# Kernel tuning notes

Hardware: AMD Instinct MI355X
Metric: run time of the kernel (lower is better)

## Reference

```python
import jax, jax.numpy as jnp
import numpy as np

N_NODES = 50000
N_EDGES = 500000
CLIP_DIM = 512   # openai/clip-vit-base-patch32 projection_dim
HIDDEN = 512
NUM_CLASSES = 100


def setup_inputs() -> dict:
    key = jax.random.key(0)
    ks = jax.random.split(key, 8)
    x = jax.random.normal(ks[0], (N_NODES, CLIP_DIM), dtype=jnp.float32)
    edge_index = jax.random.randint(ks[1], (2, N_EDGES), 0, N_NODES)
    W1 = jax.random.normal(ks[2], (HIDDEN, CLIP_DIM), dtype=jnp.float32) / np.sqrt(CLIP_DIM)
    b1 = jnp.zeros((HIDDEN,), dtype=jnp.float32)
    W2 = jax.random.normal(ks[3], (HIDDEN, HIDDEN), dtype=jnp.float32) / np.sqrt(HIDDEN)
    b2 = jnp.zeros((HIDDEN,), dtype=jnp.float32)
    Wc = jax.random.normal(ks[4], (NUM_CLASSES, HIDDEN), dtype=jnp.float32) / np.sqrt(HIDDEN)
    bc = jnp.zeros((NUM_CLASSES,), dtype=jnp.float32)
    return {"x": x, "edge_index": edge_index, "W1": W1, "b1": b1,
            "W2": W2, "b2": b2, "Wc": Wc, "bc": bc}


def _gcn_conv(h, W, b, src, dst, coef, n_nodes):
    # PyG GCNConv: transform, then normalized scatter-add aggregation, then bias.
    h = h @ W.T                                   # [N, out]
    msg = h[src] * coef[:, None]                  # [E+N, out] gathered messages
    out = jax.ops.segment_sum(msg, dst, num_segments=n_nodes)
    return out + b


def reference(x, edge_index, W1, b1, W2, b2, Wc, bc):
    n = x.shape[0]
    loop = jnp.arange(n, dtype=edge_index.dtype)
    src = jnp.concatenate([edge_index[0], loop])  # add self-loops (GCN default)
    dst = jnp.concatenate([edge_index[1], loop])
    # symmetric normalization deg^-1/2 on both endpoints (unit edge weights)
    deg = jax.ops.segment_sum(jnp.ones_like(src, dtype=x.dtype), dst, num_segments=n)
    norm = jax.lax.rsqrt(deg)                     # deg >= 1 due to self-loops
    coef = norm[src] * norm[dst]

    h = _gcn_conv(x, W1, b1, src, dst, coef, n)
    h = jax.nn.relu(h)
    # dropout(p=0.2) is identity in eval mode
    h = _gcn_conv(h, W2, b2, src, dst, coef, n)
    h = jax.nn.relu(h)
    return h @ Wc.T + bc                          # [N, num_classes]
```

## Files before the change

### kernel.cpp

```cpp
#include <hip/hip_runtime.h>

#define HIDDEN 512
#define BLK_ELEMS (64 * 128 * 8)

typedef __attribute__((ext_vector_type(8))) short short8;
typedef __attribute__((ext_vector_type(4))) float f32x4;

__device__ __forceinline__ unsigned short f2bf(float f) {
    unsigned u = __float_as_uint(f);
    unsigned r = (u + 0x7FFFu + ((u >> 16) & 1u)) >> 16;
    return (unsigned short)r;
}
__device__ __forceinline__ float bf2f(unsigned short h) {
    return __uint_as_float(((unsigned)h) << 16);
}

__device__ __forceinline__ void load_lds16(const unsigned short* g, unsigned short* l) {
    __builtin_amdgcn_global_load_lds(
        (const __attribute__((address_space(1))) unsigned int*)(g),
        (__attribute__((address_space(3))) unsigned int*)(l), 16, 0, 0);
}

__device__ __forceinline__ void acc8(uint4 v, float cf, float* a) {
    a[0] = fmaf(cf, bf2f((unsigned short)(v.x & 0xFFFF)), a[0]);
    a[1] = fmaf(cf, bf2f((unsigned short)(v.x >> 16)),    a[1]);
    a[2] = fmaf(cf, bf2f((unsigned short)(v.y & 0xFFFF)), a[2]);
    a[3] = fmaf(cf, bf2f((unsigned short)(v.y >> 16)),    a[3]);
    a[4] = fmaf(cf, bf2f((unsigned short)(v.z & 0xFFFF)), a[4]);
    a[5] = fmaf(cf, bf2f((unsigned short)(v.z >> 16)),    a[5]);
    a[6] = fmaf(cf, bf2f((unsigned short)(v.w & 0xFFFF)), a[6]);
    a[7] = fmaf(cf, bf2f((unsigned short)(v.w >> 16)),    a[7]);
}


__device__ __forceinline__ void cast_chunk(const float* __restrict__ src,
                                           unsigned short* __restrict__ dst,
                                           int rows, int o) {
    int blk = o >> 13;
    int rem = o & 8191;
    int g = rem >> 7;
    int m = rem & 127;
    int row = blk * 128 + m;
    short8 v;
    if (row < rows) {
        const float* p = src + (size_t)row * HIDDEN + g * 8;
        float4 f0 = *(const float4*)p;
        float4 f1 = *(const float4*)(p + 4);
        v[0] = (short)f2bf(f0.x); v[1] = (short)f2bf(f0.y);
        v[2] = (short)f2bf(f0.z); v[3] = (short)f2bf(f0.w);
        v[4] = (short)f2bf(f1.x); v[5] = (short)f2bf(f1.y);
        v[6] = (short)f2bf(f1.z); v[7] = (short)f2bf(f1.w);
    } else {
        v = (short8)0;
    }
    *(short8*)(dst + (size_t)o * 8) = v;
}


__global__ __launch_bounds__(256)
void fused_count_castx(const int* __restrict__ dstv, int* __restrict__ cnt, int E, int countB,
                       const float* __restrict__ x, unsigned short* __restrict__ bufA,
                       int rows, int xchunks) {
    int b = blockIdx.x;
    if (b < countB) {
        int e = b * 256 + threadIdx.x;
        if (e < E) atomicAdd(&cnt[dstv[e]], 1);
    } else {
        int o = (b - countB) * 256 + threadIdx.x;
        if (o < xchunks) cast_chunk(x, bufA, rows, o);
    }
}


__global__ __launch_bounds__(256)
void fused_bsum_castw(const int* __restrict__ cnt, float* __restrict__ norm,
                      int* __restrict__ bsums, int n, int NSB,
                      const float* __restrict__ W1, const float* __restrict__ W2,
                      const float* __restrict__ Wc,
                      unsigned short* __restrict__ W1t, unsigned short* __restrict__ W2t,
                      unsigned short* __restrict__ Wct, int NC) {
    __shared__ int red[256];
    int tid = threadIdx.x;
    if ((int)blockIdx.x < NSB) {
        int i = blockIdx.x * 256 + tid;
        int v = 0;
        if (i < n) {
            v = cnt[i];
            norm[i] = rsqrtf((float)(v + 1));
        }
        red[tid] = v;
        __syncthreads();
        #pragma unroll
        for (int off = 128; off > 0; off >>= 1) {
            if (tid < off) red[tid] += red[tid + off];
            __syncthreads();
        }
        if (tid == 0) bsums[blockIdx.x] = red[0];
    } else {
        int o = ((int)blockIdx.x - NSB) * 256 + tid;
        if (o < 32768) {
            cast_chunk(W1, W1t, HIDDEN, o);
        } else if (o < 65536) {
            cast_chunk(W2, W2t, HIDDEN, o - 32768);
        } else if (o < 73728) {
            cast_chunk(Wc, Wct, NC, o - 65536);
        }
    }
}

__global__ __launch_bounds__(256)
void bscan_kernel(const int* __restrict__ bsums, int* __restrict__ boffs,
                  int* __restrict__ rowptr_n, int nb) {
    __shared__ int buf[256];
    int tid = threadIdx.x;
    int v = (tid < nb) ? bsums[tid] : 0;
    buf[tid] = v;
    __syncthreads();
    #pragma unroll
    for (int off = 1; off < 256; off <<= 1) {
        int t = (tid >= off) ? buf[tid - off] : 0;
        __syncthreads();
        buf[tid] += t;
        __syncthreads();
    }
    if (tid < nb) boffs[tid] = buf[tid] - v;
    if (tid == 255) rowptr_n[0] = buf[255];
}

__global__ __launch_bounds__(256)
void scan_final_kernel(const int* __restrict__ cnt, const int* __restrict__ boffs,
                       int* __restrict__ rowptr, int* __restrict__ cursor, int n) {
    __shared__ int buf[256];
    int tid = threadIdx.x;
    int i = blockIdx.x * 256 + tid;
    int v = (i < n) ? cnt[i] : 0;
    buf[tid] = v;
    __syncthreads();
    #pragma unroll
    for (int off = 1; off < 256; off <<= 1) {
        int t = (tid >= off) ? buf[tid - off] : 0;
        __syncthreads();
        buf[tid] += t;
        __syncthreads();
    }
    if (i < n) {
        int ex = boffs[blockIdx.x] + buf[tid] - v;
        rowptr[i] = ex;
        cursor[i] = ex;
    }
}


template<int MODE>
__device__ __forceinline__ void gemm_body(const unsigned short* __restrict__ At,
                                          const unsigned short* __restrict__ Bt,
                                          const float* __restrict__ bias,
                                          void* __restrict__ Cout,
                                          int M, int NC, int mb, int nb) {
    __shared__ __align__(16) unsigned short As[8 * 128 * 8];
    __shared__ __align__(16) unsigned short Bs[8 * 128 * 8];

    const int tid = threadIdx.x;
    const int wid = tid >> 6;
    const int lane = tid & 63;
    const int wm = wid & 1, wn = wid >> 1;
    const int lm = lane & 15;
    const int lq = lane >> 4;

    const unsigned short* Ab = At + (size_t)mb * BLK_ELEMS;
    const unsigned short* Bb = Bt + (size_t)nb * BLK_ELEMS;

    f32x4 acc[4][4];
    #pragma unroll
    for (int i = 0; i < 4; ++i)
        #pragma unroll
        for (int j = 0; j < 4; ++j) acc[i][j] = (f32x4)0.f;

    for (int kt = 0; kt < 8; ++kt) {
        __syncthreads();
        const unsigned short* ga = Ab + kt * (8 * 1024);
        const unsigned short* gb = Bb + kt * (8 * 1024);
        #pragma unroll
        for (int i = 0; i < 4; ++i) {
            int off = (tid + i * 256) * 8;
            load_lds16(ga + off, As + off);
            load_lds16(gb + off, Bs + off);
        }
        __syncthreads();
        #pragma unroll
        for (int ks = 0; ks < 2; ++ks) {
            int g = ks * 4 + lq;
            int base = g * 1024 + lm * 8;
            short8 af[4], bfr[4];
            #pragma unroll
            for (int mt = 0; mt < 4; ++mt)
                af[mt] = *(const short8*)&As[base + (wm * 64 + mt * 16) * 8];
            #pragma unroll
            for (int nt = 0; nt < 4; ++nt)
                bfr[nt] = *(const short8*)&Bs[base + (wn * 64 + nt * 16) * 8];
            #pragma unroll
            for (int mt = 0; mt < 4; ++mt)
                #pragma unroll
                for (int nt = 0; nt < 4; ++nt)
                    acc[mt][nt] = __builtin_amdgcn_mfma_f32_16x16x32_bf16(
                        af[mt], bfr[nt], acc[mt][nt], 0, 0, 0);
        }
    }

    #pragma unroll
    for (int mt = 0; mt < 4; ++mt) {
        #pragma unroll
        for (int nt = 0; nt < 4; ++nt) {
            int col = nb * 128 + wn * 64 + nt * 16 + lm;
            f32x4 v = acc[mt][nt];
            #pragma unroll
            for (int r = 0; r < 4; ++r) {
                int row = mb * 128 + wm * 64 + mt * 16 + lq * 4 + r;
                if (row < M) {
                    if (MODE == 0) {
                        ((unsigned short*)Cout)[(size_t)row * HIDDEN + col] = f2bf(v[r]);
                    } else {
                        if (col < NC)
                            ((float*)Cout)[(size_t)row * NC + col] = v[r] + bias[col];
                    }
                }
            }
        }
    }
}

__device__ __forceinline__ bool swz_decode(int bid, int NB, int& mb, int& nb) {
    int p = bid & 7;
    int s = bid >> 3;
    nb = s & 3;
    mb = (s >> 2) * 8 + p;
    return mb < NB;
}

template<int MODE>
__global__ __launch_bounds__(256)
void gemm_swz(const unsigned short* __restrict__ At, const unsigned short* __restrict__ Bt,
              const float* __restrict__ bias, void* __restrict__ Cout,
              int M, int NC, int NB) {
    int mb, nb;
    if (!swz_decode(blockIdx.x, NB, mb, nb)) return;
    gemm_body<MODE>(At, Bt, bias, Cout, M, NC, mb, nb);
}

template<int MODE>
__global__ __launch_bounds__(256)
void gemm_plain(const unsigned short* __restrict__ At, const unsigned short* __restrict__ Bt,
                const float* __restrict__ bias, void* __restrict__ Cout,
                int M, int NC) {
    gemm_body<MODE>(At, Bt, bias, Cout, M, NC, blockIdx.x, blockIdx.y);
}


__global__ __launch_bounds__(256)
void fused_fill_gemm1(const int* __restrict__ src, const int* __restrict__ dstv,
                      const float* __restrict__ norm, int* __restrict__ cursor,
                      int2* __restrict__ epair, int E, int fillB,
                      const unsigned short* __restrict__ At, const unsigned short* __restrict__ Bt,
                      void* __restrict__ Cout, int M, int NB) {
    int b = blockIdx.x;
    if (b < fillB) {
        int e = b * 256 + threadIdx.x;
        if (e < E) {
            int s = src[e], d = dstv[e];
            float cf = norm[s] * norm[d];
            int p = atomicAdd(&cursor[d], 1);
            epair[p] = make_int2(s, __float_as_int(cf));
        }
    } else {
        int mb, nb;
        if (swz_decode(b - fillB, NB, mb, nb))
            gemm_body<0>(At, Bt, nullptr, Cout, M, HIDDEN, mb, nb);
    }
}


__global__ __launch_bounds__(256)
void aggregate_kernel(const unsigned short* __restrict__ h, const int* __restrict__ rowptr,
                      const int2* __restrict__ epair, const float* __restrict__ norm,
                      const float* __restrict__ bias, unsigned short* __restrict__ out_t,
                      int N) {
    const int wave = threadIdx.x >> 6;
    const int lane = threadIdx.x & 63;
    const int node = blockIdx.x * 4 + wave;
    if (node >= N) return;
    const uint4* h4 = (const uint4*)h;
    const int c = lane;

    float a[8];
    {
        uint4 sv = h4[(size_t)node * 64 + c];
        float nv = norm[node];
        float invd = nv * nv;
        a[0] = a[1] = a[2] = a[3] = a[4] = a[5] = a[6] = a[7] = 0.f;
        acc8(sv, invd, a);
    }

    int beg = rowptr[node], end = rowptr[node + 1];
    int j = beg;
    if ((j & 1) && j < end) {
        int2 p = epair[j];
        uint4 v = h4[(size_t)p.x * 64 + c];
        acc8(v, __int_as_float(p.y), a);
        ++j;
    }
    for (; j + 8 <= end; j += 8) {
        int4 q0 = *(const int4*)(epair + j);
        int4 q1 = *(const int4*)(epair + j + 2);
        int4 q2 = *(const int4*)(epair + j + 4);
        int4 q3 = *(const int4*)(epair + j + 6);
        uint4 v0 = h4[(size_t)q0.x * 64 + c];
        uint4 v1 = h4[(size_t)q0.z * 64 + c];
        uint4 v2 = h4[(size_t)q1.x * 64 + c];
        uint4 v3 = h4[(size_t)q1.z * 64 + c];
        uint4 v4 = h4[(size_t)q2.x * 64 + c];
        uint4 v5 = h4[(size_t)q2.z * 64 + c];
        uint4 v6 = h4[(size_t)q3.x * 64 + c];
        uint4 v7 = h4[(size_t)q3.z * 64 + c];
        acc8(v0, __int_as_float(q0.y), a);
        acc8(v1, __int_as_float(q0.w), a);
        acc8(v2, __int_as_float(q1.y), a);
        acc8(v3, __int_as_float(q1.w), a);
        acc8(v4, __int_as_float(q2.y), a);
        acc8(v5, __int_as_float(q2.w), a);
        acc8(v6, __int_as_float(q3.y), a);
        acc8(v7, __int_as_float(q3.w), a);
    }
    for (; j < end; ++j) {
        int2 p = epair[j];
        uint4 v = h4[(size_t)p.x * 64 + c];
        acc8(v, __int_as_float(p.y), a);
    }

    const float4 b0 = *(const float4*)(bias + c * 8);
    const float4 b1 = *(const float4*)(bias + c * 8 + 4);
    a[0] = fmaxf(a[0] + b0.x, 0.f); a[1] = fmaxf(a[1] + b0.y, 0.f);
    a[2] = fmaxf(a[2] + b0.z, 0.f); a[3] = fmaxf(a[3] + b0.w, 0.f);
    a[4] = fmaxf(a[4] + b1.x, 0.f); a[5] = fmaxf(a[5] + b1.y, 0.f);
    a[6] = fmaxf(a[6] + b1.z, 0.f); a[7] = fmaxf(a[7] + b1.w, 0.f);

    size_t off = (size_t)(node >> 7) * BLK_ELEMS + (size_t)c * 1024 + (node & 127) * 8;
    uint4 o;
    o.x = (unsigned)f2bf(a[0]) | ((unsigned)f2bf(a[1]) << 16);
    o.y = (unsigned)f2bf(a[2]) | ((unsigned)f2bf(a[3]) << 16);
    o.z = (unsigned)f2bf(a[4]) | ((unsigned)f2bf(a[5]) << 16);
    o.w = (unsigned)f2bf(a[6]) | ((unsigned)f2bf(a[7]) << 16);
    *(uint4*)(out_t + off) = o;
}


extern "C" void kernel_launch(void* const* d_in, const int* in_sizes, int n_in,
                              void* d_out, int out_size, void* d_ws, size_t ws_size,
                              hipStream_t stream) {
    const float* x  = (const float*)d_in[0];
    const int*   ei = (const int*)d_in[1];
    const float* W1 = (const float*)d_in[2];
    const float* b1 = (const float*)d_in[3];
    const float* W2 = (const float*)d_in[4];
    const float* b2 = (const float*)d_in[5];
    const float* Wc = (const float*)d_in[6];
    const float* bc = (const float*)d_in[7];

    const int N  = in_sizes[0] / HIDDEN;
    const int E  = in_sizes[1] / 2;
    const int NC = in_sizes[6] / HIDDEN;
    const int NB = (N + 127) / 128;
    const int NSB = (N + 255) / 256;

    const int* src = ei;
    const int* dst = ei + E;

    char* ws = (char*)d_ws;
    int*   cnt    = (int*)(ws);
    int*   rowptr = (int*)(ws + (256 << 10));
    int*   cursor = (int*)(ws + (512 << 10));
    float* normv  = (float*)(ws + (768 << 10));
    int*   bsums  = (int*)(ws + (968 << 10));
    int*   boffs  = (int*)(ws + (990 << 10));
    int2*  epair  = (int2*)(ws + (1ull << 20));
    unsigned short* W1t = (unsigned short*)(ws + (6ull << 20));
    unsigned short* W2t = (unsigned short*)(ws + (6ull << 20) + (512 << 10));
    unsigned short* Wct = (unsigned short*)(ws + (7ull << 20));
    unsigned short* bufA = (unsigned short*)(ws + (16ull << 20));
    unsigned short* bufB = (unsigned short*)(ws + (80ull << 20));
    unsigned short* hbuf = (unsigned short*)(ws + (144ull << 20));

    const int countB = (E + 255) / 256;
    const int xchunks = NB * 8192;
    const int castxB = (xchunks + 255) / 256;
    const int gemmB = 8 * 4 * ((NB + 7) / 8);

    hipMemsetAsync(cnt, 0, N * sizeof(int), stream);
    fused_count_castx<<<countB + castxB, 256, 0, stream>>>(dst, cnt, E, countB,
                                                           x, bufA, N, xchunks);
    fused_bsum_castw<<<NSB + 288, 256, 0, stream>>>(cnt, normv, bsums, N, NSB,
                                                    W1, W2, Wc, W1t, W2t, Wct, NC);
    bscan_kernel<<<1, 256, 0, stream>>>(bsums, boffs, rowptr + N, NSB);
    scan_final_kernel<<<NSB, 256, 0, stream>>>(cnt, boffs, rowptr, cursor, N);
    fused_fill_gemm1<<<countB + gemmB, 256, 0, stream>>>(src, dst, normv, cursor, epair,
                                                         E, countB,
                                                         bufA, W1t, hbuf, N, NB);
    aggregate_kernel<<<(N + 3) / 4, 256, 0, stream>>>(hbuf, rowptr, epair, normv, b1, bufB, N);
    gemm_swz<0><<<gemmB, 256, 0, stream>>>(bufB, W2t, nullptr, hbuf, N, HIDDEN, NB);
    aggregate_kernel<<<(N + 3) / 4, 256, 0, stream>>>(hbuf, rowptr, epair, normv, b2, bufA, N);
    gemm_plain<1><<<dim3(NB, 1), 256, 0, stream>>>(bufA, Wct, bc, d_out, N, NC);
}
```

Baseline: 514.1 us.

## Split aggregation into column passes with edges spread across wave sub-slots

The GCN aggregation kernel is restructured so each wave handles one 128-column slice of a node (grid y = 4 passes). The four 16-lane groups in the wave take interleaved edges and are reduced with cross-lane shuffles. The aim is to shrink each pass's gathered working set so it fits in cache better, and to add memory-level parallelism per node. In exchange there are four times as many blocks, rowptr/epair are reread per pass, and the shuffle reduction and partial-lane writes add overhead.

Measured after the change: 524.5 us. 1.02x slower.

```diff
diff --git a/kernel.cpp b/kernel.cpp
--- a/kernel.cpp
+++ b/kernel.cpp
@@ -280,76 +280,66 @@
 
 
 __global__ __launch_bounds__(256)
-void aggregate_kernel(const unsigned short* __restrict__ h, const int* __restrict__ rowptr,
-                      const int2* __restrict__ epair, const float* __restrict__ norm,
-                      const float* __restrict__ bias, unsigned short* __restrict__ out_t,
-                      int N) {
+void aggregate_pass_kernel(const unsigned short* __restrict__ h, const int* __restrict__ rowptr,
+                           const int2* __restrict__ epair, const float* __restrict__ norm,
+                           const float* __restrict__ bias, unsigned short* __restrict__ out_t,
+                           int N) {
     const int wave = threadIdx.x >> 6;
     const int lane = threadIdx.x & 63;
+    const int slot = lane >> 4;
+    const int q    = lane & 15;
     const int node = blockIdx.x * 4 + wave;
+    const int pass = blockIdx.y;
     if (node >= N) return;
-    const uint4* h4 = (const uint4*)h;
-    const int c = lane;
-
-    float a[8];
-    {
-        uint4 sv = h4[(size_t)node * 64 + c];
-        float nv = norm[node];
-        float invd = nv * nv;
-        a[0] = a[1] = a[2] = a[3] = a[4] = a[5] = a[6] = a[7] = 0.f;
-        acc8(sv, invd, a);
-    }
-
-    int beg = rowptr[node], end = rowptr[node + 1];
-    int j = beg;
-    if ((j & 1) && j < end) {
-        int2 p = epair[j];
-        uint4 v = h4[(size_t)p.x * 64 + c];
-        acc8(v, __int_as_float(p.y), a);
-        ++j;
-    }
-    for (; j + 8 <= end; j += 8) {
-        int4 q0 = *(const int4*)(epair + j);
-        int4 q1 = *(const int4*)(epair + j + 2);
-        int4 q2 = *(const int4*)(epair + j + 4);
-        int4 q3 = *(const int4*)(epair + j + 6);
-        uint4 v0 = h4[(size_t)q0.x * 64 + c];
-        uint4 v1 = h4[(size_t)q0.z * 64 + c];
-        uint4 v2 = h4[(size_t)q1.x * 64 + c];
-        uint4 v3 = h4[(size_t)q1.z * 64 + c];
-        uint4 v4 = h4[(size_t)q2.x * 64 + c];
-        uint4 v5 = h4[(size_t)q2.z * 64 + c];
-        uint4 v6 = h4[(size_t)q3.x * 64 + c];
-        uint4 v7 = h4[(size_t)q3.z * 64 + c];
-        acc8(v0, __int_as_float(q0.y), a);
-        acc8(v1, __int_as_float(q0.w), a);
-        acc8(v2, __int_as_float(q1.y), a);
-        acc8(v3, __int_as_float(q1.w), a);
-        acc8(v4, __int_as_float(q2.y), a);
-        acc8(v5, __int_as_float(q2.w), a);
-        acc8(v6, __int_as_float(q3.y), a);
-        acc8(v7, __int_as_float(q3.w), a);
-    }
-    for (; j < end; ++j) {
-        int2 p = epair[j];
-        uint4 v = h4[(size_t)p.x * 64 + c];
-        acc8(v, __int_as_float(p.y), a);
-    }
-
-    const float4 b0 = *(const float4*)(bias + c * 8);
-    const float4 b1 = *(const float4*)(bias + c * 8 + 4);
-    a[0] = fmaxf(a[0] + b0.x, 0.f); a[1] = fmaxf(a[1] + b0.y, 0.f);
-    a[2] = fmaxf(a[2] + b0.z, 0.f); a[3] = fmaxf(a[3] + b0.w, 0.f);
-    a[4] = fmaxf(a[4] + b1.x, 0.f); a[5] = fmaxf(a[5] + b1.y, 0.f);
-    a[6] = fmaxf(a[6] + b1.z, 0.f); a[7] = fmaxf(a[7] + b1.w, 0.f);
-
-    size_t off = (size_t)(node >> 7) * BLK_ELEMS + (size_t)c * 1024 + (node & 127) * 8;
-    uint4 o;
-    o.x = (unsigned)f2bf(a[0]) | ((unsigned)f2bf(a[1]) << 16);
-    o.y = (unsigned)f2bf(a[2]) | ((unsigned)f2bf(a[3]) << 16);
-    o.z = (unsigned)f2bf(a[4]) | ((unsigned)f2bf(a[5]) << 16);
-    o.w = (unsigned)f2bf(a[6]) | ((unsigned)f2bf(a[7]) << 16);
-    *(uint4*)(out_t + off) = o;
+
+    const int col0 = pass * 128 + q * 8;
+    const unsigned short* hbase = h + col0;
+
+    float a[8] = {0.f, 0.f, 0.f, 0.f, 0.f, 0.f, 0.f, 0.f};
+    float nv = norm[node];
+    if (slot == 0) {
+        uint4 sv = *(const uint4*)(hbase + (size_t)node * HIDDEN);
+        acc8(sv, nv * nv, a);
+    }
+
+    const int beg = rowptr[node], end = rowptr[node + 1];
+    int j = beg + slot;
+    for (; j + 4 < end; j += 8) {
+        int2 p0 = epair[j];
+        int2 p1 = epair[j + 4];
+        uint4 v0 = *(const uint4*)(hbase + (size_t)p0.x * HIDDEN);
+        uint4 v1 = *(const uint4*)(hbase + (size_t)p1.x * HIDDEN);
+        acc8(v0, __int_as_float(p0.y), a);
+        acc8(v1, __int_as_float(p1.y), a);
+    }
+    if (j < end) {
+        int2 p0 = epair[j];
+        uint4 v0 = *(const uint4*)(hbase + (size_t)p0.x * HIDDEN);
+        acc8(v0, __int_as_float(p0.y), a);
+    }
+
+    #pragma unroll
+    for (int k = 0; k < 8; ++k) {
+        a[k] += __shfl_xor(a[k], 16, 64);
+        a[k] += __shfl_xor(a[k], 32, 64);
+    }
+
+    if (slot == 0) {
+        const float4 b0 = *(const float4*)(bias + col0);
+        const float4 b1 = *(const float4*)(bias + col0 + 4);
+        a[0] = fmaxf(a[0] + b0.x, 0.f); a[1] = fmaxf(a[1] + b0.y, 0.f);
+        a[2] = fmaxf(a[2] + b0.z, 0.f); a[3] = fmaxf(a[3] + b0.w, 0.f);
+        a[4] = fmaxf(a[4] + b1.x, 0.f); a[5] = fmaxf(a[5] + b1.y, 0.f);
+        a[6] = fmaxf(a[6] + b1.z, 0.f); a[7] = fmaxf(a[7] + b1.w, 0.f);
+        size_t off = (size_t)(node >> 7) * BLK_ELEMS + (size_t)(pass * 16 + q) * 1024
+                   + (size_t)(node & 127) * 8;
+        uint4 o;
+        o.x = (unsigned)f2bf(a[0]) | ((unsigned)f2bf(a[1]) << 16);
+        o.y = (unsigned)f2bf(a[2]) | ((unsigned)f2bf(a[3]) << 16);
+        o.z = (unsigned)f2bf(a[4]) | ((unsigned)f2bf(a[5]) << 16);
+        o.w = (unsigned)f2bf(a[6]) | ((unsigned)f2bf(a[7]) << 16);
+        *(uint4*)(out_t + off) = o;
+    }
 }
 
 
@@ -404,8 +394,9 @@
     fused_fill_gemm1<<<countB + gemmB, 256, 0, stream>>>(src, dst, normv, cursor, epair,
                                                          E, countB,
                                                          bufA, W1t, hbuf, N, NB);
-    aggregate_kernel<<<(N + 3) / 4, 256, 0, stream>>>(hbuf, rowptr, epair, normv, b1, bufB, N);
+    dim3 gagg((N + 3) / 4, 4);
+    aggregate_pass_kernel<<<gagg, 256, 0, stream>>>(hbuf, rowptr, epair, normv, b1, bufB, N);
     gemm_swz<0><<<gemmB, 256, 0, stream>>>(bufB, W2t, nullptr, hbuf, N, HIDDEN, NB);
-    aggregate_kernel<<<(N + 3) / 4, 256, 0, stream>>>(hbuf, rowptr, epair, normv, b2, bufA, N);
+    aggregate_pass_kernel<<<gagg, 256, 0, stream>>>(hbuf, rowptr, epair, normv, b2, bufA, N);
     gemm_plain<1><<<dim3(NB, 1), 256, 0, stream>>>(bufA, Wct, bc, d_out, N, NC);
 }
```
